# Optimization experiments

Measured on AMD Instinct MI355X. Metric: run time of the kernel, lower is better.

Reference implementation:

```python
import jax, jax.numpy as jnp
import numpy as np

B, S, D, H = 4, 2048, 1024, 16
HD = D // H  # head dim = 64

def setup_inputs() -> dict:
    key = jax.random.key(0)
    ks = jax.random.split(key, 6)
    scale = 0.02
    x = jax.random.normal(ks[0], (B, S, D), dtype=jnp.float32)
    Wq = jax.random.normal(ks[1], (D, D), dtype=jnp.float32) * scale
    Wk = jax.random.normal(ks[2], (D, D), dtype=jnp.float32) * scale
    Wv = jax.random.normal(ks[3], (D, D), dtype=jnp.float32) * scale
    Wo = jax.random.normal(ks[4], (D, D), dtype=jnp.float32) * scale
    bo = jnp.zeros((D,), dtype=jnp.float32)
    return {"x": x, "Wq": Wq, "Wk": Wk, "Wv": Wv, "Wo": Wo, "bo": bo}

def reference(x, Wq, Wk, Wv, Wo, bo):
    b, s, d = x.shape
    h, hd = H, HD
    # project and split heads -> [b, h, s, hd]
    def split_heads(t):
        return t.reshape(b, s, h, hd).transpose(0, 2, 1, 3)
    q = split_heads(x @ Wq)
    k = split_heads(x @ Wk)
    v = split_heads(x @ Wv)
    # causal attention with full score matrix (faithful to the naive impl)
    scores = jnp.einsum('bhqd,bhkd->bhqk', q, k)
    causal = jnp.triu(jnp.ones((s, s), dtype=bool), k=1)  # True above diagonal
    scores = jnp.where(causal, -jnp.inf, scores)
    attn = jax.nn.softmax(scores / jnp.sqrt(jnp.float32(hd)), axis=-1)
    ctx = jnp.einsum('bhqk,bhkd->bhqd', attn, v)
    ctx = ctx.transpose(0, 2, 1, 3).reshape(b, s, d)
    return ctx @ Wo + bo
```

## Files before the change

### kernel.cpp

```cpp
#include <hip/hip_runtime.h>
#include <math.h>
#include <stdint.h>

typedef __bf16 bf16;
typedef bf16 bf16x2 __attribute__((ext_vector_type(2)));
typedef bf16 bf16x8 __attribute__((ext_vector_type(8)));
typedef short s16x4 __attribute__((ext_vector_type(4)));
typedef float floatx4 __attribute__((ext_vector_type(4)));

static constexpr int Sq = 2048, Dm = 1024, Hh = 16, HDim = 64;

#define GAS __attribute__((address_space(1)))
#define LAS __attribute__((address_space(3)))

__device__ __forceinline__ void dma16(const void* g, void* l) {
    __builtin_amdgcn_global_load_lds((const GAS void*)g, (LAS void*)l, 16, 0, 0);
}

__device__ __forceinline__ uint32_t pk_bf16(float a, float b) {
    bf16x2 t;
    t[0] = (bf16)a;
    t[1] = (bf16)b;
    return __builtin_bit_cast(uint32_t, t);
}

__global__ __launch_bounds__(256)
void prep_all(const float* __restrict__ Wq, const float* __restrict__ Wk,
              const float* __restrict__ Wv, const float* __restrict__ Wo,
              bf16* __restrict__ Wt,
              const float* __restrict__ x, bf16* __restrict__ xb)
{
    const int t = threadIdx.x;
    if (blockIdx.z == 4) {
        const int b = blockIdx.y * 16 + blockIdx.x;
        const size_t base = ((size_t)b * 256 + t) * 8;
#pragma unroll
        for (int it = 0; it < 16; it++) {
            const size_t i = base + (size_t)it * 524288;
            float4 f0 = *(const float4*)(x + i);
            float4 f1 = *(const float4*)(x + i + 4);
            bf16x8 v;
            v[0]=(bf16)f0.x; v[1]=(bf16)f0.y; v[2]=(bf16)f0.z; v[3]=(bf16)f0.w;
            v[4]=(bf16)f1.x; v[5]=(bf16)f1.y; v[6]=(bf16)f1.z; v[7]=(bf16)f1.w;
            *(bf16x8*)(xb + i) = v;
        }
        return;
    }
    const int w = blockIdx.z;
    const float* W = (w == 0) ? Wq : (w == 1) ? Wk : (w == 2) ? Wv : Wo;
    bf16* dst = Wt + (size_t)w * 1024 * 1024;
    const int k0 = blockIdx.x * 64, n0 = blockIdx.y * 64;
    __shared__ uint32_t Tl[64][33];
    {
        const int c8 = (t & 7) * 8;
        const int kp = t >> 3;
        const float* r0 = W + (size_t)(k0 + 2 * kp) * 1024 + n0 + c8;
        const float* r1 = r0 + 1024;
        float4 a0 = *(const float4*)r0, a1 = *(const float4*)(r0 + 4);
        float4 b0 = *(const float4*)r1, b1 = *(const float4*)(r1 + 4);
        float ra[8] = {a0.x, a0.y, a0.z, a0.w, a1.x, a1.y, a1.z, a1.w};
        float rb[8] = {b0.x, b0.y, b0.z, b0.w, b1.x, b1.y, b1.z, b1.w};
#pragma unroll
        for (int j = 0; j < 8; j++)
            Tl[c8 + j][kp] = pk_bf16(ra[j], rb[j]);
    }
    __syncthreads();
    {
        const int c = t >> 2, dq = (t & 3) * 8;
        uint32_t d[8];
#pragma unroll
        for (int i = 0; i < 8; i++) d[i] = Tl[c][dq + i];
        uint32_t* o = (uint32_t*)(dst + (size_t)(n0 + c) * 1024 + k0 + dq * 2);
        *(uint4*)o       = make_uint4(d[0], d[1], d[2], d[3]);
        *(uint4*)(o + 4) = make_uint4(d[4], d[5], d[6], d[7]);
    }
}

template <int AMODE>
__global__ __launch_bounds__(256, 2)
void qkv_gemm(const float* __restrict__ x, const bf16* __restrict__ xb,
              const bf16* __restrict__ Wt,
              bf16* __restrict__ Qb, bf16* __restrict__ Kb, bf16* __restrict__ VT)
{
    const int zz = blockIdx.z;
    const bf16* Wsel = Wt + (size_t)zz * 1024 * 1024;

    __shared__ __align__(16) unsigned char smem[34816];
    bf16 (*As1)[64] = (bf16(*)[64])smem;
    bf16 (*As0)[72] = (bf16(*)[72])smem;
    bf16 (*Bs)[64]  = (bf16(*)[64])(smem + (AMODE ? 16384 : 18432));

    const int tid  = threadIdx.x;
    const int wave = tid >> 6, lane = tid & 63, quad = lane >> 4, l16 = lane & 15;
    const int bm = blockIdx.x * 128, bn = blockIdx.y * 128;
    const int wm = (wave >> 1) * 64, wn = (wave & 1) * 64;

    floatx4 acc[4][4];
#pragma unroll
    for (int i = 0; i < 4; i++)
#pragma unroll
        for (int j = 0; j < 4; j++) acc[i][j] = (floatx4){0.f, 0.f, 0.f, 0.f};

    for (int k0 = 0; k0 < 1024; k0 += 64) {
        __syncthreads();
#pragma unroll
        for (int i = 0; i < 4; i++) {
            const int row = wave * 32 + i * 8 + (lane >> 3);
            const int lb  = (lane & 7) ^ (row & 7);
            const bf16* g = Wsel + (size_t)(bn + row) * 1024 + k0 + lb * 8;
            dma16((const void*)g, (void*)&Bs[wave * 32 + i * 8][0]);
        }
        if (AMODE) {
#pragma unroll
            for (int i = 0; i < 4; i++) {
                const int row = wave * 32 + i * 8 + (lane >> 3);
                const int lb  = (lane & 7) ^ (row & 7);
                const bf16* g = xb + (size_t)(bm + row) * 1024 + k0 + lb * 8;
                dma16((const void*)g, (void*)&As1[wave * 32 + i * 8][0]);
            }
        } else {
#pragma unroll
            for (int it = 0; it < 2; it++) {
                const int r  = (tid >> 2) + it * 64;
                const int cq = (tid & 3) * 16;
                const float* src = x + (size_t)(bm + r) * 1024 + k0 + cq;
                float4 f0 = *(const float4*)src,       f1 = *(const float4*)(src + 4);
                float4 f2 = *(const float4*)(src + 8), f3 = *(const float4*)(src + 12);
                bf16x8 v0, v1;
                v0[0]=(bf16)f0.x; v0[1]=(bf16)f0.y; v0[2]=(bf16)f0.z; v0[3]=(bf16)f0.w;
                v0[4]=(bf16)f1.x; v0[5]=(bf16)f1.y; v0[6]=(bf16)f1.z; v0[7]=(bf16)f1.w;
                v1[0]=(bf16)f2.x; v1[1]=(bf16)f2.y; v1[2]=(bf16)f2.z; v1[3]=(bf16)f2.w;
                v1[4]=(bf16)f3.x; v1[5]=(bf16)f3.y; v1[6]=(bf16)f3.z; v1[7]=(bf16)f3.w;
                *(bf16x8*)&As0[r][cq]     = v0;
                *(bf16x8*)&As0[r][cq + 8] = v1;
            }
        }
        __syncthreads();

#pragma unroll
        for (int kk = 0; kk < 2; kk++) {
            bf16x8 a[4], b[4];
#pragma unroll
            for (int tm = 0; tm < 4; tm++) {
                const int m = wm + tm * 16 + l16;
                if (AMODE) {
                    const int phys = (kk * 4 + quad) ^ (m & 7);
                    a[tm] = *(const bf16x8*)&As1[m][phys * 8];
                } else {
                    a[tm] = *(const bf16x8*)&As0[m][kk * 32 + quad * 8];
                }
            }
#pragma unroll
            for (int tn = 0; tn < 4; tn++) {
                const int n = wn + tn * 16 + l16;
                const int phys = (kk * 4 + quad) ^ (n & 7);
                b[tn] = *(const bf16x8*)&Bs[n][phys * 8];
            }
#pragma unroll
            for (int tm = 0; tm < 4; tm++)
#pragma unroll
                for (int tn = 0; tn < 4; tn++)
                    acc[tm][tn] = __builtin_amdgcn_mfma_f32_16x16x32_bf16(a[tm], b[tn], acc[tm][tn], 0, 0, 0);
        }
    }

    if (zz < 2) {
        bf16* dst = (zz == 0) ? Qb : Kb;
        const float sc = (zz == 1) ? 0.18033688f : 1.0f;
#pragma unroll
        for (int tm = 0; tm < 4; tm++)
#pragma unroll
            for (int tn = 0; tn < 4; tn++)
#pragma unroll
                for (int r = 0; r < 4; r++) {
                    const int m = bm + wm + tm * 16 + quad * 4 + r;
                    const int n = bn + wn + tn * 16 + l16;
                    const int bb = m >> 11, s = m & 2047;
                    const int h = n >> 6, d = n & 63;
                    dst[(((size_t)(bb * Hh + h)) * Sq + s) * HDim + d] = (bf16)(acc[tm][tn][r] * sc);
                }
    } else {
        __syncthreads();
        bf16 (*CT)[136] = (bf16(*)[136])smem;
#pragma unroll
        for (int tm = 0; tm < 4; tm++)
#pragma unroll
            for (int tn = 0; tn < 4; tn++)
#pragma unroll
                for (int r = 0; r < 4; r++) {
                    const int ml = wm + tm * 16 + quad * 4 + r;
                    const int nl = wn + tn * 16 + l16;
                    const int pml = (ml & 0x43) | ((ml & 0x30) >> 2) | ((ml & 0x0C) << 2);
                    CT[nl][pml] = (bf16)acc[tm][tn][r];
                }
        __syncthreads();
        const int nl = tid >> 1, part = tid & 1;
        const int n = bn + nl, h = n >> 6, d = n & 63;
        const int bbv = bm >> 11, s0v = bm & 2047;
        bf16* o = VT + (((size_t)(bbv * Hh + h)) * HDim + d) * Sq + s0v + part * 64;
#pragma unroll
        for (int i = 0; i < 8; i++)
            *(bf16x8*)(o + i * 8) = *(const bf16x8*)&CT[nl][part * 64 + i * 8];
    }
}

__global__ __launch_bounds__(256, 4)
void attn(const bf16* __restrict__ Qb, const bf16* __restrict__ Kb,
          const bf16* __restrict__ VTg, bf16* __restrict__ Cx)
{
    const int bh = blockIdx.x;
    const int bl = bh >> 4, h = bh & 15;

    __shared__ __align__(16) bf16 Kl[2][64][64];
    __shared__ __align__(16) bf16 Vt[2][64][64];

    const int tid  = threadIdx.x;
    const int wave = tid >> 6, lane = tid & 63, quad = lane >> 4, l16 = lane & 15;

    const int srow = wave * 16 + (lane >> 3);
    const int lb   = (lane & 7) ^ (lane >> 3);

    for (int pass = 0; pass < 2; pass++) {
        const int qt = (pass == 0) ? (int)blockIdx.y : 31 - (int)blockIdx.y;
        const int q0 = qt * 64;
        const int nk = qt + 1;

        bf16x8 bq[2];
        {
            const bf16* Qrow = Qb + ((size_t)bh * Sq + q0 + wave * 16 + l16) * HDim;
            bq[0] = *(const bf16x8*)(Qrow + quad * 8);
            bq[1] = *(const bf16x8*)(Qrow + 32 + quad * 8);
        }

        floatx4 acc[4];
#pragma unroll
        for (int i = 0; i < 4; i++) acc[i] = (floatx4){0.f, 0.f, 0.f, 0.f};
        float l_part = 0.f;

        const bf16* kp = Kb  + ((size_t)bh * Sq + srow) * HDim + lb * 8;
        const bf16* vp = VTg + ((size_t)bh * HDim + srow) * Sq + lb * 8;

        auto stage = [&](int nb) {
#pragma unroll
            for (int i = 0; i < 2; i++) {
                dma16((const void*)(kp + (size_t)(i * 8) * HDim), (void*)&Kl[nb][wave * 16 + i * 8][0]);
                dma16((const void*)(vp + (size_t)(i * 8) * Sq),  (void*)&Vt[nb][wave * 16 + i * 8][0]);
            }
            kp += 64 * HDim;
            vp += 64;
        };

        auto tile = [&](int nb, bool masked) {
            const bf16 (*Ksm)[64] = Kl[nb];
            const bf16 (*Vsm)[64] = Vt[nb];

            floatx4 sT[4];
            __builtin_amdgcn_s_setprio(1);
#pragma unroll
            for (int mt = 0; mt < 4; mt++) {
                const int kr = mt * 16 + l16;
                bf16x8 ak0 = *(const bf16x8*)&Ksm[kr][(quad ^ (kr & 7)) * 8];
                bf16x8 ak1 = *(const bf16x8*)&Ksm[kr][((4 + quad) ^ (kr & 7)) * 8];
                floatx4 z = (floatx4){0.f, 0.f, 0.f, 0.f};
                z = __builtin_amdgcn_mfma_f32_16x16x32_bf16(ak0, bq[0], z, 0, 0, 0);
                z = __builtin_amdgcn_mfma_f32_16x16x32_bf16(ak1, bq[1], z, 0, 0, 0);
                sT[mt] = z;
            }
            __builtin_amdgcn_s_setprio(0);

            if (masked) {
#pragma unroll
                for (int mt = 0; mt < 4; mt++)
#pragma unroll
                    for (int r = 0; r < 4; r++) {
                        const int keyl  = mt * 16 + quad * 4 + r;
                        const int qrowl = wave * 16 + l16;
                        if (keyl > qrowl) sT[mt][r] = -1e30f;
                    }
            }

            s16x4 pb[4];
            {
                float rs = 0.f;
#pragma unroll
                for (int mt = 0; mt < 4; mt++) {
#pragma unroll
                    for (int r = 0; r < 4; r++) {
                        const float e = __builtin_amdgcn_exp2f(sT[mt][r]);
                        sT[mt][r] = e;
                        rs += e;
                    }
                    const uint2 pk = make_uint2(pk_bf16(sT[mt][0], sT[mt][1]),
                                                pk_bf16(sT[mt][2], sT[mt][3]));
                    pb[mt] = __builtin_bit_cast(s16x4, pk);
                }
                l_part += rs;
            }

            __builtin_amdgcn_s_setprio(1);
#pragma unroll
            for (int db = 0; db < 4; db++) {
                const int row = db * 16 + l16;
#pragma unroll
                for (int p = 0; p < 2; p++) {
                    const int phys = ((quad * 2 + p) ^ (row & 7)) * 16;
                    const uint4 v = *(const uint4*)((const char*)&Vsm[row][0] + phys);
                    const s16x4 av0 = __builtin_bit_cast(s16x4, make_uint2(v.x, v.y));
                    const s16x4 av1 = __builtin_bit_cast(s16x4, make_uint2(v.z, v.w));
                    acc[db] = __builtin_amdgcn_mfma_f32_16x16x16bf16_1k(av0, pb[2 * p],     acc[db], 0, 0, 0);
                    acc[db] = __builtin_amdgcn_mfma_f32_16x16x16bf16_1k(av1, pb[2 * p + 1], acc[db], 0, 0, 0);
                }
            }
            __builtin_amdgcn_s_setprio(0);
        };

        stage(0);
        for (int kt = 0; kt < nk - 1; kt++) {
            const int cur = kt & 1;
            stage(cur ^ 1);
            asm volatile("s_waitcnt vmcnt(4)" ::: "memory");
            __builtin_amdgcn_s_barrier();
            tile(cur, false);
            __builtin_amdgcn_s_barrier();
        }
        asm volatile("s_waitcnt vmcnt(0)" ::: "memory");
        __builtin_amdgcn_s_barrier();
        tile((nk - 1) & 1, true);
        __builtin_amdgcn_s_barrier();

        {
            float rs = l_part;
            rs += __shfl_xor(rs, 16, 64);
            rs += __shfl_xor(rs, 32, 64);
            const float inv = __builtin_amdgcn_rcpf(rs);
            const int qrow = q0 + wave * 16 + l16;
#pragma unroll
            for (int db = 0; db < 4; db++) {
                uint2 pk;
                pk.x = pk_bf16(acc[db][0] * inv, acc[db][1] * inv);
                pk.y = pk_bf16(acc[db][2] * inv, acc[db][3] * inv);
                *(uint2*)(Cx + ((size_t)(bl * Sq + qrow)) * Dm + h * HDim + db * 16 + quad * 4) = pk;
            }
        }
    }
}

__global__ __launch_bounds__(256, 2)
void out_gemm(const bf16* __restrict__ Cx, const bf16* __restrict__ WtO,
              const float* __restrict__ bo, float* __restrict__ out, int mbase)
{
    __shared__ __align__(16) bf16 As2[128][64];
    __shared__ __align__(16) bf16 Bs2[128][64];

    const int tid  = threadIdx.x;
    const int wave = tid >> 6, lane = tid & 63, quad = lane >> 4, l16 = lane & 15;
    const int bm = blockIdx.x * 128, bn = blockIdx.y * 128;
    const int wm = (wave >> 1) * 64, wn = (wave & 1) * 64;

    floatx4 acc[4][4];
#pragma unroll
    for (int i = 0; i < 4; i++)
#pragma unroll
        for (int j = 0; j < 4; j++) acc[i][j] = (floatx4){0.f, 0.f, 0.f, 0.f};

    for (int k0 = 0; k0 < 1024; k0 += 64) {
        __syncthreads();
#pragma unroll
        for (int i = 0; i < 4; i++) {
            const int row = wave * 32 + i * 8 + (lane >> 3);
            const int lb  = (lane & 7) ^ (row & 7);
            const bf16* ga = Cx  + (size_t)(bm + row) * 1024 + k0 + lb * 8;
            const bf16* gb = WtO + (size_t)(bn + row) * 1024 + k0 + lb * 8;
            dma16((const void*)ga, (void*)&As2[wave * 32 + i * 8][0]);
            dma16((const void*)gb, (void*)&Bs2[wave * 32 + i * 8][0]);
        }
        __syncthreads();

#pragma unroll
        for (int kk = 0; kk < 2; kk++) {
            bf16x8 a[4], b[4];
#pragma unroll
            for (int tm = 0; tm < 4; tm++) {
                const int m = wm + tm * 16 + l16;
                const int phys = (kk * 4 + quad) ^ (m & 7);
                a[tm] = *(const bf16x8*)&As2[m][phys * 8];
            }
#pragma unroll
            for (int tn = 0; tn < 4; tn++) {
                const int n = wn + tn * 16 + l16;
                const int phys = (kk * 4 + quad) ^ (n & 7);
                b[tn] = *(const bf16x8*)&Bs2[n][phys * 8];
            }
#pragma unroll
            for (int tm = 0; tm < 4; tm++)
#pragma unroll
                for (int tn = 0; tn < 4; tn++)
                    acc[tm][tn] = __builtin_amdgcn_mfma_f32_16x16x32_bf16(a[tm], b[tn], acc[tm][tn], 0, 0, 0);
        }
    }

#pragma unroll
    for (int tm = 0; tm < 4; tm++)
#pragma unroll
        for (int tn = 0; tn < 4; tn++)
#pragma unroll
            for (int r = 0; r < 4; r++) {
                const int m = bm + wm + tm * 16 + quad * 4 + r;
                const int n = bn + wn + tn * 16 + l16;
                out[(size_t)(mbase + m) * 1024 + n] = acc[tm][tn][r] + bo[n];
            }
}

extern "C" void kernel_launch(void* const* d_in, const int* in_sizes, int n_in,
                              void* d_out, int out_size, void* d_ws, size_t ws_size,
                              hipStream_t stream)
{
    const float* x  = (const float*)d_in[0];
    const float* Wq = (const float*)d_in[1];
    const float* Wk = (const float*)d_in[2];
    const float* Wv = (const float*)d_in[3];
    const float* Wo = (const float*)d_in[4];
    const float* bo = (const float*)d_in[5];
    float* out = (float*)d_out;

    const size_t M1 = 1024 * 1024;
    const size_t XE = (size_t)8192 * 1024;

    if (ws_size >= (size_t)72 * 1024 * 1024) {
        bf16* Wt = (bf16*)d_ws;
        bf16* xb = Wt + 4 * M1;
        bf16* Qb = xb + XE;
        bf16* Kb = Qb + XE;
        bf16* VT = Kb + XE;
        bf16* Cx = xb;

        prep_all<<<dim3(16, 16, 5), 256, 0, stream>>>(Wq, Wk, Wv, Wo, Wt, x, xb);
        qkv_gemm<1><<<dim3(64, 8, 3), 256, 0, stream>>>(x, xb, Wt, Qb, Kb, VT);
        attn<<<dim3(64, 16), 256, 0, stream>>>(Qb, Kb, VT, Cx);
        out_gemm<<<dim3(64, 8), 256, 0, stream>>>(Cx, Wt + 3 * M1, bo, out, 0);
    } else {
        bf16* Wt = (bf16*)d_ws;
        bf16* Qb = Wt + 4 * M1;
        bf16* Kb = Qb + XE;
        bf16* VT = Kb + XE;
        bf16* Cx = VT + XE;

        prep_all<<<dim3(16, 16, 4), 256, 0, stream>>>(Wq, Wk, Wv, Wo, Wt, nullptr, nullptr);
        qkv_gemm<0><<<dim3(64, 8, 3), 256, 0, stream>>>(x, nullptr, Wt, Qb, Kb, VT);
        const size_t chunk = (size_t)2 * Hh * Sq * HDim;
        for (int c = 0; c < 2; c++) {
            attn<<<dim3(32, 16), 256, 0, stream>>>(Qb + c * chunk, Kb + c * chunk,
                                                   VT + c * chunk, Cx);
            out_gemm<<<dim3(32, 8), 256, 0, stream>>>(Cx, Wt + 3 * M1, bo, out, c * 4096);
        }
    }
}
```

Measured before the change: 230.4 us.

## Fuse paired query tiles into one KV sweep sharing K/V loads

The attention kernel used to process its two query tiles (qt and 31-qt) in two separate passes, each streaming K/V from key tile 0. It now runs a single sweep over key tiles and computes both query tiles against each staged K/V tile while tile A is still active. This roughly halves K/V global loads and LDS staging for the shared prefix, and gives each tile's MFMA work more independent instructions. In exchange register pressure rises from doubled accumulators and Q fragments under launch_bounds(256,4), which could cause spills or lower occupancy.

```diff
diff --git a/kernel.cpp b/kernel.cpp
--- a/kernel.cpp
+++ b/kernel.cpp
@@ -210,6 +210,8 @@
 {
     const int bh = blockIdx.x;
     const int bl = bh >> 4, h = bh & 15;
+    const int qtA = (int)blockIdx.y;
+    const int qtB = 31 - qtA;
 
     __shared__ __align__(16) bf16 Kl[2][64][64];
     __shared__ __align__(16) bf16 Vt[2][64][64];
@@ -220,129 +222,175 @@
     const int srow = wave * 16 + (lane >> 3);
     const int lb   = (lane & 7) ^ (lane >> 3);
 
-    for (int pass = 0; pass < 2; pass++) {
-        const int qt = (pass == 0) ? (int)blockIdx.y : 31 - (int)blockIdx.y;
-        const int q0 = qt * 64;
-        const int nk = qt + 1;
-
-        bf16x8 bq[2];
+    bf16x8 bqA[2], bqB[2];
+    {
+        const bf16* QA = Qb + ((size_t)bh * Sq + qtA * 64 + wave * 16 + l16) * HDim;
+        bqA[0] = *(const bf16x8*)(QA + quad * 8);
+        bqA[1] = *(const bf16x8*)(QA + 32 + quad * 8);
+        const bf16* QB = Qb + ((size_t)bh * Sq + qtB * 64 + wave * 16 + l16) * HDim;
+        bqB[0] = *(const bf16x8*)(QB + quad * 8);
+        bqB[1] = *(const bf16x8*)(QB + 32 + quad * 8);
+    }
+
+    floatx4 accA[4], accB[4];
+#pragma unroll
+    for (int i = 0; i < 4; i++) {
+        accA[i] = (floatx4){0.f, 0.f, 0.f, 0.f};
+        accB[i] = (floatx4){0.f, 0.f, 0.f, 0.f};
+    }
+    float lA = 0.f, lB = 0.f;
+
+    const bf16* kp = Kb  + ((size_t)bh * Sq + srow) * HDim + lb * 8;
+    const bf16* vp = VTg + ((size_t)bh * HDim + srow) * Sq + lb * 8;
+
+    auto stage = [&](int nb) {
+#pragma unroll
+        for (int i = 0; i < 2; i++) {
+            dma16((const void*)(kp + (size_t)(i * 8) * HDim), (void*)&Kl[nb][wave * 16 + i * 8][0]);
+            dma16((const void*)(vp + (size_t)(i * 8) * Sq),  (void*)&Vt[nb][wave * 16 + i * 8][0]);
+        }
+        kp += 64 * HDim;
+        vp += 64;
+    };
+
+    auto tile = [&](int nb, bool doA, bool maskA, bool maskB) {
+        const bf16 (*Ksm)[64] = Kl[nb];
+        const bf16 (*Vsm)[64] = Vt[nb];
+
+        floatx4 sA[4], sB[4];
+        __builtin_amdgcn_s_setprio(1);
+#pragma unroll
+        for (int mt = 0; mt < 4; mt++) {
+            const int kr = mt * 16 + l16;
+            bf16x8 ak0 = *(const bf16x8*)&Ksm[kr][(quad ^ (kr & 7)) * 8];
+            bf16x8 ak1 = *(const bf16x8*)&Ksm[kr][((4 + quad) ^ (kr & 7)) * 8];
+            if (doA) {
+                floatx4 z = (floatx4){0.f, 0.f, 0.f, 0.f};
+                z = __builtin_amdgcn_mfma_f32_16x16x32_bf16(ak0, bqA[0], z, 0, 0, 0);
+                z = __builtin_amdgcn_mfma_f32_16x16x32_bf16(ak1, bqA[1], z, 0, 0, 0);
+                sA[mt] = z;
+            }
+            floatx4 z = (floatx4){0.f, 0.f, 0.f, 0.f};
+            z = __builtin_amdgcn_mfma_f32_16x16x32_bf16(ak0, bqB[0], z, 0, 0, 0);
+            z = __builtin_amdgcn_mfma_f32_16x16x32_bf16(ak1, bqB[1], z, 0, 0, 0);
+            sB[mt] = z;
+        }
+        __builtin_amdgcn_s_setprio(0);
+
+        if (maskA) {
+#pragma unroll
+            for (int mt = 0; mt < 4; mt++)
+#pragma unroll
+                for (int r = 0; r < 4; r++)
+                    if (mt * 16 + quad * 4 + r > wave * 16 + l16) sA[mt][r] = -1e30f;
+        }
+        if (maskB) {
+#pragma unroll
+            for (int mt = 0; mt < 4; mt++)
+#pragma unroll
+                for (int r = 0; r < 4; r++)
+                    if (mt * 16 + quad * 4 + r > wave * 16 + l16) sB[mt][r] = -1e30f;
+        }
+
+        s16x4 pbA[4], pbB[4];
+        if (doA) {
+            float rs = 0.f;
+#pragma unroll
+            for (int mt = 0; mt < 4; mt++) {
+#pragma unroll
+                for (int r = 0; r < 4; r++) {
+                    const float e = __builtin_amdgcn_exp2f(sA[mt][r]);
+                    sA[mt][r] = e;
+                    rs += e;
+                }
+                const uint2 pk = make_uint2(pk_bf16(sA[mt][0], sA[mt][1]),
+                                            pk_bf16(sA[mt][2], sA[mt][3]));
+                pbA[mt] = __builtin_bit_cast(s16x4, pk);
+            }
+            lA += rs;
+        }
         {
-            const bf16* Qrow = Qb + ((size_t)bh * Sq + q0 + wave * 16 + l16) * HDim;
-            bq[0] = *(const bf16x8*)(Qrow + quad * 8);
-            bq[1] = *(const bf16x8*)(Qrow + 32 + quad * 8);
-        }
-
-        floatx4 acc[4];
-#pragma unroll
-        for (int i = 0; i < 4; i++) acc[i] = (floatx4){0.f, 0.f, 0.f, 0.f};
-        float l_part = 0.f;
-
-        const bf16* kp = Kb  + ((size_t)bh * Sq + srow) * HDim + lb * 8;
-        const bf16* vp = VTg + ((size_t)bh * HDim + srow) * Sq + lb * 8;
-
-        auto stage = [&](int nb) {
-#pragma unroll
-            for (int i = 0; i < 2; i++) {
-                dma16((const void*)(kp + (size_t)(i * 8) * HDim), (void*)&Kl[nb][wave * 16 + i * 8][0]);
-                dma16((const void*)(vp + (size_t)(i * 8) * Sq),  (void*)&Vt[nb][wave * 16 + i * 8][0]);
-            }
-            kp += 64 * HDim;
-            vp += 64;
-        };
-
-        auto tile = [&](int nb, bool masked) {
-            const bf16 (*Ksm)[64] = Kl[nb];
-            const bf16 (*Vsm)[64] = Vt[nb];
-
-            floatx4 sT[4];
-            __builtin_amdgcn_s_setprio(1);
+            float rs = 0.f;
 #pragma unroll
             for (int mt = 0; mt < 4; mt++) {
-                const int kr = mt * 16 + l16;
-                bf16x8 ak0 = *(const bf16x8*)&Ksm[kr][(quad ^ (kr & 7)) * 8];
-                bf16x8 ak1 = *(const bf16x8*)&Ksm[kr][((4 + quad) ^ (kr & 7)) * 8];
-                floatx4 z = (floatx4){0.f, 0.f, 0.f, 0.f};
-                z = __builtin_amdgcn_mfma_f32_16x16x32_bf16(ak0, bq[0], z, 0, 0, 0);
-                z = __builtin_amdgcn_mfma_f32_16x16x32_bf16(ak1, bq[1], z, 0, 0, 0);
-                sT[mt] = z;
-            }
-            __builtin_amdgcn_s_setprio(0);
-
-            if (masked) {
-#pragma unroll
-                for (int mt = 0; mt < 4; mt++)
-#pragma unroll
-                    for (int r = 0; r < 4; r++) {
-                        const int keyl  = mt * 16 + quad * 4 + r;
-                        const int qrowl = wave * 16 + l16;
-                        if (keyl > qrowl) sT[mt][r] = -1e30f;
-                    }
-            }
-
-            s16x4 pb[4];
-            {
-                float rs = 0.f;
-#pragma unroll
-                for (int mt = 0; mt < 4; mt++) {
-#pragma unroll
-                    for (int r = 0; r < 4; r++) {
-                        const float e = __builtin_amdgcn_exp2f(sT[mt][r]);
-                        sT[mt][r] = e;
-                        rs += e;
-                    }
-                    const uint2 pk = make_uint2(pk_bf16(sT[mt][0], sT[mt][1]),
-                                                pk_bf16(sT[mt][2], sT[mt][3]));
-                    pb[mt] = __builtin_bit_cast(s16x4, pk);
+#pragma unroll
+                for (int r = 0; r < 4; r++) {
+                    const float e = __builtin_amdgcn_exp2f(sB[mt][r]);
+                    sB[mt][r] = e;
+                    rs += e;
                 }
-                l_part += rs;
-            }
-
-            __builtin_amdgcn_s_setprio(1);
-#pragma unroll
-            for (int db = 0; db < 4; db++) {
-                const int row = db * 16 + l16;
-#pragma unroll
-                for (int p = 0; p < 2; p++) {
-                    const int phys = ((quad * 2 + p) ^ (row & 7)) * 16;
-                    const uint4 v = *(const uint4*)((const char*)&Vsm[row][0] + phys);
-                    const s16x4 av0 = __builtin_bit_cast(s16x4, make_uint2(v.x, v.y));
-                    const s16x4 av1 = __builtin_bit_cast(s16x4, make_uint2(v.z, v.w));
-                    acc[db] = __builtin_amdgcn_mfma_f32_16x16x16bf16_1k(av0, pb[2 * p],     acc[db], 0, 0, 0);
-                    acc[db] = __builtin_amdgcn_mfma_f32_16x16x16bf16_1k(av1, pb[2 * p + 1], acc[db], 0, 0, 0);
+                const uint2 pk = make_uint2(pk_bf16(sB[mt][0], sB[mt][1]),
+                                            pk_bf16(sB[mt][2], sB[mt][3]));
+                pbB[mt] = __builtin_bit_cast(s16x4, pk);
+            }
+            lB += rs;
+        }
+
+        __builtin_amdgcn_s_setprio(1);
+#pragma unroll
+        for (int db = 0; db < 4; db++) {
+            const int row = db * 16 + l16;
+#pragma unroll
+            for (int p = 0; p < 2; p++) {
+                const int phys = ((quad * 2 + p) ^ (row & 7)) * 16;
+                const uint4 v = *(const uint4*)((const char*)&Vsm[row][0] + phys);
+                const s16x4 av0 = __builtin_bit_cast(s16x4, make_uint2(v.x, v.y));
+                const s16x4 av1 = __builtin_bit_cast(s16x4, make_uint2(v.z, v.w));
+                if (doA) {
+                    accA[db] = __builtin_amdgcn_mfma_f32_16x16x16bf16_1k(av0, pbA[2 * p],     accA[db], 0, 0, 0);
+                    accA[db] = __builtin_amdgcn_mfma_f32_16x16x16bf16_1k(av1, pbA[2 * p + 1], accA[db], 0, 0, 0);
                 }
-            }
-            __builtin_amdgcn_s_setprio(0);
-        };
-
-        stage(0);
-        for (int kt = 0; kt < nk - 1; kt++) {
-            const int cur = kt & 1;
-            stage(cur ^ 1);
-            asm volatile("s_waitcnt vmcnt(4)" ::: "memory");
-            __builtin_amdgcn_s_barrier();
-            tile(cur, false);
-            __builtin_amdgcn_s_barrier();
-        }
-        asm volatile("s_waitcnt vmcnt(0)" ::: "memory");
+                accB[db] = __builtin_amdgcn_mfma_f32_16x16x16bf16_1k(av0, pbB[2 * p],     accB[db], 0, 0, 0);
+                accB[db] = __builtin_amdgcn_mfma_f32_16x16x16bf16_1k(av1, pbB[2 * p + 1], accB[db], 0, 0, 0);
+            }
+        }
+        __builtin_amdgcn_s_setprio(0);
+    };
+
+    stage(0);
+    int kt = 0;
+    for (; kt < qtA; ++kt) {
+        stage((kt & 1) ^ 1);
+        asm volatile("s_waitcnt vmcnt(4)" ::: "memory");
         __builtin_amdgcn_s_barrier();
-        tile((nk - 1) & 1, true);
+        tile(kt & 1, true, false, false);
         __builtin_amdgcn_s_barrier();
-
-        {
-            float rs = l_part;
-            rs += __shfl_xor(rs, 16, 64);
-            rs += __shfl_xor(rs, 32, 64);
-            const float inv = __builtin_amdgcn_rcpf(rs);
-            const int qrow = q0 + wave * 16 + l16;
-#pragma unroll
-            for (int db = 0; db < 4; db++) {
-                uint2 pk;
-                pk.x = pk_bf16(acc[db][0] * inv, acc[db][1] * inv);
-                pk.y = pk_bf16(acc[db][2] * inv, acc[db][3] * inv);
-                *(uint2*)(Cx + ((size_t)(bl * Sq + qrow)) * Dm + h * HDim + db * 16 + quad * 4) = pk;
-            }
-        }
-    }
+    }
+    {
+        stage((kt & 1) ^ 1);
+        asm volatile("s_waitcnt vmcnt(4)" ::: "memory");
+        __builtin_amdgcn_s_barrier();
+        tile(kt & 1, true, true, false);
+        __builtin_amdgcn_s_barrier();
+        ++kt;
+    }
+    for (; kt < qtB; ++kt) {
+        stage((kt & 1) ^ 1);
+        asm volatile("s_waitcnt vmcnt(4)" ::: "memory");
+        __builtin_amdgcn_s_barrier();
+        tile(kt & 1, false, false, false);
+        __builtin_amdgcn_s_barrier();
+    }
+    asm volatile("s_waitcnt vmcnt(0)" ::: "memory");
+    __builtin_amdgcn_s_barrier();
+    tile(kt & 1, false, false, true);
+
+    auto writeO = [&](const floatx4* acc, float lp, int qt) {
+        float rs = lp;
+        rs += __shfl_xor(rs, 16, 64);
+        rs += __shfl_xor(rs, 32, 64);
+        const float inv = __builtin_amdgcn_rcpf(rs);
+        const int qrow = qt * 64 + wave * 16 + l16;
+#pragma unroll
+        for (int db = 0; db < 4; db++) {
+            uint2 pk;
+            pk.x = pk_bf16(acc[db][0] * inv, acc[db][1] * inv);
+            pk.y = pk_bf16(acc[db][2] * inv, acc[db][3] * inv);
+            *(uint2*)(Cx + ((size_t)(bl * Sq + qrow)) * Dm + h * HDim + db * 16 + quad * 4) = pk;
+        }
+    };
+    writeO(accA, lA, qtA);
+    writeO(accB, lB, qtB);
 }
 
 __global__ __launch_bounds__(256, 2)
```

After: 230.8 us. Within noise of the previous version (+0.2%).

## Double attention query tile to 128 rows with 8 waves sharing K/V tiles

Applied to the files above, without the earlier changes.

The attention kernel now uses 512-thread blocks covering 128 query rows instead of 64, so each staged 64-key K/V tile is shared by eight waves rather than four. Each thread issues one async global-to-LDS load per K and V tile, and the loop is split into unmasked tiles plus two diagonal tiles masked with a key offset. The aim is to halve K/V global and LDS staging traffic per query row and amortise barriers. The cost is more waves meeting at each barrier, and the lower four waves spend a full tile of compute on keys that are entirely masked on the last diagonal tile.

```diff
diff --git a/kernel.cpp b/kernel.cpp
--- a/kernel.cpp
+++ b/kernel.cpp
@@ -204,7 +204,7 @@
     }
 }
 
-__global__ __launch_bounds__(256, 4)
+__global__ __launch_bounds__(512, 2)
 void attn(const bf16* __restrict__ Qb, const bf16* __restrict__ Kb,
           const bf16* __restrict__ VTg, bf16* __restrict__ Cx)
 {
@@ -217,13 +217,13 @@
     const int tid  = threadIdx.x;
     const int wave = tid >> 6, lane = tid & 63, quad = lane >> 4, l16 = lane & 15;
 
-    const int srow = wave * 16 + (lane >> 3);
+    const int srow = wave * 8 + (lane >> 3);
     const int lb   = (lane & 7) ^ (lane >> 3);
 
     for (int pass = 0; pass < 2; pass++) {
-        const int qt = (pass == 0) ? (int)blockIdx.y : 31 - (int)blockIdx.y;
-        const int q0 = qt * 64;
-        const int nk = qt + 1;
+        const int qt = (pass == 0) ? (int)blockIdx.y : 15 - (int)blockIdx.y;
+        const int q0 = qt * 128;
+        const int nt = 2 * qt + 2;
 
         bf16x8 bq[2];
         {
@@ -241,16 +241,13 @@
         const bf16* vp = VTg + ((size_t)bh * HDim + srow) * Sq + lb * 8;
 
         auto stage = [&](int nb) {
-#pragma unroll
-            for (int i = 0; i < 2; i++) {
-                dma16((const void*)(kp + (size_t)(i * 8) * HDim), (void*)&Kl[nb][wave * 16 + i * 8][0]);
-                dma16((const void*)(vp + (size_t)(i * 8) * Sq),  (void*)&Vt[nb][wave * 16 + i * 8][0]);
-            }
+            dma16((const void*)kp, (void*)&Kl[nb][wave * 8][0]);
+            dma16((const void*)vp, (void*)&Vt[nb][wave * 8][0]);
             kp += 64 * HDim;
             vp += 64;
         };
 
-        auto tile = [&](int nb, bool masked) {
+        auto tile = [&](int nb, int MOFF) {
             const bf16 (*Ksm)[64] = Kl[nb];
             const bf16 (*Vsm)[64] = Vt[nb];
 
@@ -268,12 +265,12 @@
             }
             __builtin_amdgcn_s_setprio(0);
 
-            if (masked) {
+            if (MOFF >= 0) {
 #pragma unroll
                 for (int mt = 0; mt < 4; mt++)
 #pragma unroll
                     for (int r = 0; r < 4; r++) {
-                        const int keyl  = mt * 16 + quad * 4 + r;
+                        const int keyl  = mt * 16 + quad * 4 + r + MOFF;
                         const int qrowl = wave * 16 + l16;
                         if (keyl > qrowl) sT[mt][r] = -1e30f;
                     }
@@ -315,17 +312,25 @@
         };
 
         stage(0);
-        for (int kt = 0; kt < nk - 1; kt++) {
-            const int cur = kt & 1;
-            stage(cur ^ 1);
-            asm volatile("s_waitcnt vmcnt(4)" ::: "memory");
+        int kt = 0;
+        for (; kt < nt - 2; ++kt) {
+            stage((kt & 1) ^ 1);
+            asm volatile("s_waitcnt vmcnt(2)" ::: "memory");
             __builtin_amdgcn_s_barrier();
-            tile(cur, false);
+            tile(kt & 1, -1);
             __builtin_amdgcn_s_barrier();
+        }
+        {
+            stage((kt & 1) ^ 1);
+            asm volatile("s_waitcnt vmcnt(2)" ::: "memory");
+            __builtin_amdgcn_s_barrier();
+            tile(kt & 1, 0);
+            __builtin_amdgcn_s_barrier();
+            ++kt;
         }
         asm volatile("s_waitcnt vmcnt(0)" ::: "memory");
         __builtin_amdgcn_s_barrier();
-        tile((nk - 1) & 1, true);
+        tile(kt & 1, 64);
         __builtin_amdgcn_s_barrier();
 
         {
@@ -436,7 +441,7 @@
 
         prep_all<<<dim3(16, 16, 5), 256, 0, stream>>>(Wq, Wk, Wv, Wo, Wt, x, xb);
         qkv_gemm<1><<<dim3(64, 8, 3), 256, 0, stream>>>(x, xb, Wt, Qb, Kb, VT);
-        attn<<<dim3(64, 16), 256, 0, stream>>>(Qb, Kb, VT, Cx);
+        attn<<<dim3(64, 8), 512, 0, stream>>>(Qb, Kb, VT, Cx);
         out_gemm<<<dim3(64, 8), 256, 0, stream>>>(Cx, Wt + 3 * M1, bo, out, 0);
     } else {
         bf16* Wt = (bf16*)d_ws;
@@ -449,8 +454,8 @@
         qkv_gemm<0><<<dim3(64, 8, 3), 256, 0, stream>>>(x, nullptr, Wt, Qb, Kb, VT);
         const size_t chunk = (size_t)2 * Hh * Sq * HDim;
         for (int c = 0; c < 2; c++) {
-            attn<<<dim3(32, 16), 256, 0, stream>>>(Qb + c * chunk, Kb + c * chunk,
-                                                   VT + c * chunk, Cx);
+            attn<<<dim3(32, 8), 512, 0, stream>>>(Qb + c * chunk, Kb + c * chunk,
+                                                  VT + c * chunk, Cx);
             out_gemm<<<dim3(32, 8), 256, 0, stream>>>(Cx, Wt + 3 * M1, bo, out, c * 4096);
         }
     }
```

After: 239.3 us. 1.04x slower.
